# Kernel optimization log

Measured on AMD Instinct MI355X. Metric: run time of the kernel, lower is better.

The kernel has to match this reference:

```python
import jax, jax.numpy as jnp
import numpy as np

EPS = 1e-6

def setup_inputs() -> dict:
    key = jax.random.key(0)
    ks = jax.random.split(key, 8)
    S, B, I, D, L = 1024, 16, 1024, 1024, 2
    std = np.sqrt(2.0 / (5.0 * I))
    inp = {
        "input": jax.random.normal(ks[0], (S, B, I), jnp.float32),
        "h0": jnp.zeros((L, B, D), jnp.float32),
        "extra0": jnp.zeros((L, B, 3 * D), jnp.float32),
        "W0": jax.random.normal(ks[1], (4 * D, I), jnp.float32) * std,
        "b0": jnp.zeros((4 * D,), jnp.float32).at[2 * D:3 * D].set(
            jax.random.uniform(ks[2], (D,), jnp.float32, 3.0, 6.0)),
        "r0": jnp.zeros((4 * D,), jnp.float32),
        "W1": jax.random.normal(ks[3], (4 * D, D), jnp.float32) * std,
        "b1": jnp.zeros((4 * D,), jnp.float32).at[2 * D:3 * D].set(
            jax.random.uniform(ks[4], (D,), jnp.float32, 3.0, 6.0)),
        "r1": jnp.zeros((4 * D,), jnp.float32),
    }
    return inp

def _cell(x, c, n, h, m, W, b, r):
    # x: (B, in), states: (B, D), W: (4D, in), b/r: (4D,)
    D = h.shape[-1]
    pre = x @ W.T + b  # (B, 4D)
    rz, ri, rf, ro = jnp.split(r, 4)
    z_pre = pre[:, 0 * D:1 * D] + rz * h
    i_pre = pre[:, 1 * D:2 * D] + ri * h
    f_pre = pre[:, 2 * D:3 * D] + rf * h
    o_pre = pre[:, 3 * D:4 * D] + ro * h
    z_t = jnp.tanh(z_pre)
    o_t = jax.nn.sigmoid(o_pre)
    m_new = jnp.maximum(f_pre + m, i_pre)
    f_t = jnp.exp(f_pre + m - m_new)
    i_t = jnp.exp(i_pre - m_new)
    c_new = f_t * c + i_t * z_t
    n_new = f_t * n + i_t
    h_new = o_t * (c_new / (jnp.abs(n_new) + EPS))
    return h_new, c_new, n_new, m_new

def _run(input, h0, extra0, params):
    D = h0.shape[-1]
    c0 = extra0[:, :, 0 * D:1 * D]
    n0 = extra0[:, :, 1 * D:2 * D]
    m0 = extra0[:, :, 2 * D:3 * D]

    def step(carry, x_t):
        h, c, n, m = carry  # each (L, B, D)
        x = x_t
        hs, cs, ns, ms = [], [], [], []
        for l, (W, b, r) in enumerate(params):
            h_new, c_new, n_new, m_new = _cell(x, c[l], n[l], h[l], m[l], W, b, r)
            hs.append(h_new); cs.append(c_new); ns.append(n_new); ms.append(m_new)
            x = h_new
        carry = (jnp.stack(hs), jnp.stack(cs), jnp.stack(ns), jnp.stack(ms))
        return carry, x

    (h_f, c_f, n_f, m_f), output = jax.lax.scan(step, (h0, c0, n0, m0), input)
    extra_f = jnp.concatenate([c_f, n_f, m_f], axis=-1)
    return output, h_f, extra_f

def reference(input, h0, extra0, W0, b0, r0, W1, b1, r1):
    params = [(W0, b0, r0), (W1, b1, r1)]
    return _run(input, h0, extra0, params)
```

## Files before the change

### kernel.cpp

```cpp
#include <hip/hip_runtime.h>
#include <hip/hip_bf16.h>

#define S_LEN  1024
#define BATCH  16
#define IDIM   1024
#define DDIM   1024
#define NG     4096
#define BD     16384
#define LAYERS 2
#define PF     16
#define PFP    8
#define NSEG   16

typedef __attribute__((ext_vector_type(8))) short   short8;
typedef __attribute__((ext_vector_type(4))) float   floatx4;
typedef __attribute__((address_space(1))) void      as1_void;
typedef __attribute__((address_space(3))) void      as3_void;

#define L2E  1.4426950408889634f
#define LN2  0.6931471805599453f

#define EXP2F(x) exp2f(x)

static __device__ __forceinline__ unsigned short f2bf(float x) {
    unsigned int u = __float_as_uint(x);
    return (unsigned short)((u + 0x7fffu + ((u >> 16) & 1u)) >> 16);
}

__global__ void detect_dtype(const void* w, int* flag)
{
    const __hip_bfloat16* p = (const __hip_bfloat16*)w;
    float mx = 0.0f;
    for (int i = threadIdx.x; i < 4096; i += 64) {
        float v = __bfloat162float(p[i]);
        float a = fabsf(v);
        if (!(a == a)) a = 1e30f;
        mx = fmaxf(mx, a);
    }
#pragma unroll
    for (int o = 32; o > 0; o >>= 1)
        mx = fmaxf(mx, __shfl_down(mx, o, 64));
    if (threadIdx.x == 0) *flag = (mx > 1e3f) ? 1 : 0;
}

__global__ void to_bf16(const void* src, size_t elem_off, const int* flag,
                        unsigned short* dst, int n)
{
    const int i = blockIdx.x * 256 + threadIdx.x;
    if (i >= n) return;
    if (*flag) dst[i] = f2bf(((const float*)src)[elem_off + i]);
    else       dst[i] = ((const unsigned short*)src)[elem_off + i];
}

__global__ void prep_small(const void* __restrict__ h0,
                           const void* __restrict__ extra0,
                           const void* __restrict__ b0s, const void* __restrict__ r0s,
                           const void* __restrict__ b1s, const void* __restrict__ r1s,
                           const int* __restrict__ flag,
                           float* __restrict__ state,
                           float* __restrict__ pb,
                           int* __restrict__ rflag)
{
    const int blk = blockIdx.x;
    const int fl = *flag;

    if (blk < 128) {
        const int idx = blk * 256 + threadIdx.x;
        const int l  = idx / BD;
        const int bd = idx % BD;
        const int b = bd >> 10, d = bd & 1023;
        float* st = state + (size_t)l * 4 * BD;
        const size_t eoff = ((size_t)l * BATCH + b) * (3 * DDIM);
        float cv, nv, mv, hv;
        if (fl) {
            const float* e = (const float*)extra0 + eoff;
            cv = e[d]; nv = e[DDIM + d]; mv = e[2 * DDIM + d];
            hv = ((const float*)h0)[(size_t)l * BD + bd];
        } else {
            const __hip_bfloat16* e = (const __hip_bfloat16*)extra0 + eoff;
            cv = __bfloat162float(e[d]);
            nv = __bfloat162float(e[DDIM + d]);
            mv = __bfloat162float(e[2 * DDIM + d]);
            hv = __bfloat162float(((const __hip_bfloat16*)h0)[(size_t)l * BD + bd]);
        }
        st[0 * BD + bd] = cv;
        st[1 * BD + bd] = nv;
        st[2 * BD + bd] = mv * L2E;
        st[3 * BD + bd] = hv;
        return;
    }

    const int which = blk - 128;
    const void* src = (which == 0) ? b0s : (which == 1) ? r0s
                    : (which == 2) ? b1s : r1s;
    float* dst = pb + (size_t)which * NG;
    int nz = 0;
#pragma unroll
    for (int j = 0; j < NG / 256; j++) {
        const int i = j * 256 + threadIdx.x;
        float v;
        if (fl) {
            v = ((const float*)src)[i];
            nz |= (v != 0.0f);
        } else {
            const unsigned short u = ((const unsigned short*)src)[i];
            nz |= ((u & 0x7fffu) != 0);
            v = __bfloat162float(((const __hip_bfloat16*)src)[i]);
        }
        dst[i] = v;
    }
    if (which == 1 || which == 3) {
        __shared__ int s[4];
        const int w = threadIdx.x >> 6;
        const int any = __any(nz) ? 1 : 0;
        if ((threadIdx.x & 63) == 0) s[w] = any;
        __syncthreads();
        if (threadIdx.x == 0) rflag[which >> 1] = !(s[0] | s[1] | s[2] | s[3]);
    }
}

__global__ __launch_bounds__(256, 2)
void gemm_bias(const __hip_bfloat16* __restrict__ A,
               const __hip_bfloat16* __restrict__ W,
               const float* __restrict__ bias,
               unsigned short* __restrict__ out,
               const int* __restrict__ rflag, int tpad)
{
    constexpr int K = 1024;
    __shared__ alignas(16) __hip_bfloat16 sA[128 * 32];
    __shared__ alignas(16) __hip_bfloat16 sB[128 * 32];

    const int t  = threadIdx.x;
    const int m0 = blockIdx.y * 128;
    const int nb = blockIdx.x;
    const int lr = t & 15;
    const int q  = (t >> 4) & 3;
    const int w  = t >> 6;
    const int wm = w >> 1, wn = w & 1;
    const int sr = t >> 2;
    const int sk = (t & 3) * 8;

    floatx4 acc[4][4] = {};

    const __hip_bfloat16* Ab = A + (size_t)(m0 + sr) * K + sk;
    const int wrow = ((sr >> 5) << 10) + nb * 32 + (sr & 31);
    const __hip_bfloat16* Wb = W + (size_t)wrow * K + sk;

    for (int k0 = 0; k0 < K; k0 += 32) {
        __syncthreads();
        __builtin_amdgcn_global_load_lds((as1_void*)(Ab + k0),            (as3_void*)&sA[sr * 32 + sk],        16, 0, 0);
        __builtin_amdgcn_global_load_lds((as1_void*)(Ab + 64 * K + k0),   (as3_void*)&sA[(sr + 64) * 32 + sk], 16, 0, 0);
        __builtin_amdgcn_global_load_lds((as1_void*)(Wb + k0),            (as3_void*)&sB[sr * 32 + sk],        16, 0, 0);
        __builtin_amdgcn_global_load_lds((as1_void*)(Wb + 2048 * K + k0), (as3_void*)&sB[(sr + 64) * 32 + sk], 16, 0, 0);
        __syncthreads();

        short8 af[4], bf[4];
#pragma unroll
        for (int i = 0; i < 4; i++)
            af[i] = *(const short8*)&sA[(wm * 64 + i * 16 + lr) * 32 + q * 8];
#pragma unroll
        for (int j = 0; j < 4; j++)
            bf[j] = *(const short8*)&sB[(j * 32 + wn * 16 + lr) * 32 + q * 8];
#pragma unroll
        for (int i = 0; i < 4; i++)
#pragma unroll
            for (int j = 0; j < 4; j++)
                acc[i][j] = __builtin_amdgcn_mfma_f32_16x16x32_bf16(af[i], bf[j], acc[i][j], 0, 0, 0);
    }

    const int d = nb * 32 + wn * 16 + lr;
    const int cl = ((nb & 1) << 5) + wn * 16 + lr;
    const int cbBase = nb >> 1;
    const float sc[4] = {2.0f * L2E, L2E, L2E, L2E};
    float bb[4];
#pragma unroll
    for (int g = 0; g < 4; g++) bb[g] = sc[g] * bias[g * 1024 + d];

    const int rfast = *rflag;

#pragma unroll
    for (int i = 0; i < 4; i++) {
#pragma unroll
        for (int reg = 0; reg < 4; reg++) {
            const int row  = m0 + wm * 64 + i * 16 + q * 4 + reg;
            const int trow = row >> 4;
            const int b    = row & 15;
            float v[4];
#pragma unroll
            for (int g = 0; g < 4; g++)
                v[g] = acc[i][g][reg] * sc[g] + bb[g];
            if (rfast) {
                const float zv = v[0];
                const float e2 = EXP2F(-fabsf(zv));
                v[0] = copysignf((1.0f - e2) * __builtin_amdgcn_rcpf(1.0f + e2), zv);
                v[3] = __builtin_amdgcn_rcpf(1.0f + EXP2F(-v[3]));
            }
            union { unsigned short us[4]; uint2 u2; } pk;
#pragma unroll
            for (int g = 0; g < 4; g++) pk.us[g] = f2bf(v[g]);
            const int cb = b * 16 + cbBase;
            *(uint2*)(out + (((size_t)cb * tpad + trow) * 64 + cl) * 4) = pk.u2;
        }
    }
}

__global__ void scan_passA(const unsigned int* __restrict__ pre,
                           const int* __restrict__ rflag,
                           float* __restrict__ smry, int T, int tpad)
{
    if (!*rflag) return;
    const int gid = blockIdx.x * 256 + threadIdx.x;
    const int chain = gid & (BD - 1);
    const int seg = gid >> 14;
    const int SEG = T / NSEG;
    const int cb = chain >> 6, cl = chain & 63;

    const uint2* p = (const uint2*)pre
                   + ((size_t)cb * tpad + seg * SEG) * 64 + cl;

    float al = 0.0f, mu = -3e38f, Bh = 0.0f, Nh = 0.0f;

    unsigned int k0[PFP], k1[PFP];
#pragma unroll
    for (int u = 0; u < PFP; u++) {
        const uint2 v = p[(size_t)u * 64];
        k0[u] = v.x; k1[u] = v.y;
    }

    for (int t = 0; t < SEG; t += PFP) {
#pragma unroll
        for (int u = 0; u < PFP; u++) {
            const float zt = __uint_as_float(k0[u] << 16);
            const float i2 = __uint_as_float(k0[u] & 0xffff0000u);
            const float f2 = __uint_as_float(k1[u] << 16);

            const uint2 nv = p[(size_t)(t + u + PFP) * 64];
            k0[u] = nv.x; k1[u] = nv.y;

            al += f2;
            const float e  = i2 - al;
            const float mn = fmaxf(mu, e);
            const float s  = EXP2F(mu - mn);
            const float ww = EXP2F(e - mn);
            Bh = fmaf(Bh, s, ww * zt);
            Nh = fmaf(Nh, s, ww);
            mu = mn;
        }
    }

    smry[0 * NSEG * BD + seg * BD + chain] = al;
    smry[1 * NSEG * BD + seg * BD + chain] = al + mu;
    smry[2 * NSEG * BD + seg * BD + chain] = Bh;
    smry[3 * NSEG * BD + seg * BD + chain] = Nh;
}

__global__ void scan_mid(float* __restrict__ smry,
                         const int* __restrict__ rflag,
                         const float* __restrict__ state, int T)
{
    if (!*rflag) return;
    const int idx = blockIdx.x * 256 + threadIdx.x;
    float c  = state[0 * BD + idx];
    float n  = state[1 * BD + idx];
    float m2 = state[2 * BD + idx];
#pragma unroll
    for (int s = 0; s < NSEG; s++) {
        const float A    = smry[0 * NSEG * BD + s * BD + idx];
        const float bmax = smry[1 * NSEG * BD + s * BD + idx];
        const float Bh   = smry[2 * NSEG * BD + s * BD + idx];
        const float Nh   = smry[3 * NSEG * BD + s * BD + idx];
        smry[0 * NSEG * BD + s * BD + idx] = c;
        smry[1 * NSEG * BD + s * BD + idx] = n;
        smry[2 * NSEG * BD + s * BD + idx] = m2;
        const float mn = fmaxf(m2 + A, bmax);
        const float sc = EXP2F(m2 + A - mn);
        const float w  = EXP2F(bmax - mn);
        c  = fmaf(sc, c, w * Bh);
        n  = fmaf(sc, n, w * Nh);
        m2 = mn;
    }
}

template<int MODE>
__global__ void scan_passB(const unsigned int* __restrict__ pre,
                           const float* __restrict__ smry,
                           const int* __restrict__ rflag,
                           float* __restrict__ state,
                           unsigned short* __restrict__ hseq,
                           void* __restrict__ gout, size_t gout_eoff,
                           const int* __restrict__ flag, int T, int tpad)
{
    if (!*rflag) return;
    const int gid = blockIdx.x * 256 + threadIdx.x;
    const int chain = gid & (BD - 1);
    const int seg = gid >> 14;
    const int SEG = T / NSEG;
    const int t0s = seg * SEG;
    const int cb = chain >> 6, cl = chain & 63;
    const int fl = *flag;

    float c  = smry[0 * NSEG * BD + seg * BD + chain];
    float n  = smry[1 * NSEG * BD + seg * BD + chain];
    float m2 = smry[2 * NSEG * BD + seg * BD + chain];

    const uint2* p = (const uint2*)pre
                   + ((size_t)cb * tpad + t0s) * 64 + cl;

    unsigned short* hb = hseq + chain + (size_t)t0s * BD;
    float*          fo = (float*)gout + gout_eoff + chain + (size_t)t0s * BD;
    unsigned short* bo = (unsigned short*)gout + gout_eoff + chain + (size_t)t0s * BD;

    float h = 0.0f;
    unsigned int k0[PFP], k1[PFP];
#pragma unroll
    for (int u = 0; u < PFP; u++) {
        const uint2 v = p[(size_t)u * 64];
        k0[u] = v.x; k1[u] = v.y;
    }

    for (int t = 0; t < SEG; t += PFP) {
#pragma unroll
        for (int u = 0; u < PFP; u++) {
            const float zt = __uint_as_float(k0[u] << 16);
            const float i2 = __uint_as_float(k0[u] & 0xffff0000u);
            const float f2 = __uint_as_float(k1[u] << 16);
            const float ot = __uint_as_float(k1[u] & 0xffff0000u);

            const uint2 nv = p[(size_t)(t + u + PFP) * 64];
            k0[u] = nv.x; k1[u] = nv.y;

            const float fm = f2 + m2;
            const float mn = fmaxf(fm, i2);
            const float ft = EXP2F(fm - mn);
            const float it = EXP2F(i2 - mn);

            c  = fmaf(ft, c, it * zt);
            n  = fmaf(ft, n, it);
            m2 = mn;
            h  = ot * c * __builtin_amdgcn_rcpf(fabsf(n) + 1e-6f);

            const size_t toff = (size_t)(t + u) * BD;
            if (MODE == 0)      hb[toff] = f2bf(h);
            else if (fl)        fo[toff] = h;
            else                bo[toff] = f2bf(h);
        }
    }

    if (seg == NSEG - 1) {
        state[0 * BD + chain] = c;
        state[1 * BD + chain] = n;
        state[2 * BD + chain] = m2;
        state[3 * BD + chain] = h;
    }
}

template<int MODE>
__global__ void slstm_scan(const unsigned int* __restrict__ pre,
                           const float* __restrict__ r,
                           float* __restrict__ state,
                           unsigned short* __restrict__ hseq,
                           void* __restrict__ gout, size_t gout_eoff,
                           const int* __restrict__ flag,
                           const int* __restrict__ rflag, int T, int tpad,
                           int pgate)
{
    const int rfast = *rflag;
    if (pgate && rfast) return;

    const int idx = blockIdx.x * 64 + threadIdx.x;
    const int d = idx & 1023;
    const int cb = idx >> 6, cl = idx & 63;
    const int fl = *flag;

    const float rz = r[d]            * (2.0f * L2E);
    const float ri = r[DDIM + d]     * L2E;
    const float rf = r[2 * DDIM + d] * L2E;
    const float ro = r[3 * DDIM + d] * L2E;

    float c  = state[0 * BD + idx];
    float n  = state[1 * BD + idx];
    float m2 = state[2 * BD + idx];
    float h  = state[3 * BD + idx];

    const uint2* p = (const uint2*)pre + (size_t)cb * tpad * 64 + cl;

    unsigned short* hb = hseq + idx;
    float*          fo = (float*)gout + gout_eoff + idx;
    unsigned short* bo = (unsigned short*)gout + gout_eoff + idx;

    unsigned int k0[PF], k1[PF];
#pragma unroll
    for (int u = 0; u < PF; u++) {
        const uint2 v = p[(size_t)u * 64];
        k0[u] = v.x; k1[u] = v.y;
    }

    if (rfast) {
        for (int t8 = 0; t8 < T; t8 += PF) {
#pragma unroll
            for (int u = 0; u < PF; u++) {
                const float zt = __uint_as_float(k0[u] << 16);
                const float i2 = __uint_as_float(k0[u] & 0xffff0000u);
                const float f2 = __uint_as_float(k1[u] << 16);
                const float ot = __uint_as_float(k1[u] & 0xffff0000u);

                const uint2 nv = p[(size_t)(t8 + u + PF) * 64];
                k0[u] = nv.x; k1[u] = nv.y;

                const float fm = f2 + m2;
                const float mn = fmaxf(fm, i2);
                const float ft = EXP2F(fm - mn);
                const float it = EXP2F(i2 - mn);

                c  = fmaf(ft, c, it * zt);
                n  = fmaf(ft, n, it);
                m2 = mn;
                h  = ot * c * __builtin_amdgcn_rcpf(fabsf(n) + 1e-6f);

                const size_t toff = (size_t)(t8 + u) * BD;
                if (MODE == 0)      hb[toff] = f2bf(h);
                else if (fl)        fo[toff] = h;
                else                bo[toff] = f2bf(h);
            }
        }
    } else {
        for (int t8 = 0; t8 < T; t8 += PF) {
#pragma unroll
            for (int u = 0; u < PF; u++) {
                float z2 = __uint_as_float(k0[u] << 16);
                float i2 = __uint_as_float(k0[u] & 0xffff0000u);
                float f2 = __uint_as_float(k1[u] << 16);
                float o2 = __uint_as_float(k1[u] & 0xffff0000u);

                const uint2 nv = p[(size_t)(t8 + u + PF) * 64];
                k0[u] = nv.x; k1[u] = nv.y;

                z2 = fmaf(rz, h, z2);
                i2 = fmaf(ri, h, i2);
                f2 = fmaf(rf, h, f2);
                o2 = fmaf(ro, h, o2);

                const float fm = f2 + m2;
                const float mn = fmaxf(fm, i2);
                const float ft = EXP2F(fm - mn);
                const float it = EXP2F(i2 - mn);

                const float e2 = EXP2F(-fabsf(z2));
                const float zt = copysignf((1.0f - e2) * __builtin_amdgcn_rcpf(1.0f + e2), z2);
                const float ot = __builtin_amdgcn_rcpf(1.0f + EXP2F(-o2));

                c  = ft * c + it * zt;
                n  = ft * n + it;
                m2 = mn;
                h  = ot * c * __builtin_amdgcn_rcpf(fabsf(n) + 1e-6f);

                const size_t toff = (size_t)(t8 + u) * BD;
                if (MODE == 0)      hb[toff] = f2bf(h);
                else if (fl)        fo[toff] = h;
                else                bo[toff] = f2bf(h);
            }
        }
    }

    state[0 * BD + idx] = c;
    state[1 * BD + idx] = n;
    state[2 * BD + idx] = m2;
    state[3 * BD + idx] = h;
}

__global__ void finalize(const float* __restrict__ state,
                         void* __restrict__ out,
                         const int* __restrict__ flag)
{
    const int idx = blockIdx.x * 256 + threadIdx.x;
    const int l  = idx / BD;
    const int bd = idx % BD;
    const int b = bd >> 10, d = bd & 1023;
    const float* st = state + (size_t)l * 4 * BD;
    const float cv = st[0 * BD + bd], nv = st[1 * BD + bd];
    const float mv = st[2 * BD + bd] * LN2;
    const float hv = st[3 * BD + bd];

    const size_t hoff = (size_t)S_LEN * BD + idx;
    const size_t eoff = (size_t)S_LEN * BD + (size_t)LAYERS * BD
                      + ((size_t)l * BATCH + b) * (3 * DDIM);
    if (*flag) {
        float* o = (float*)out;
        o[hoff] = hv;
        o[eoff + d] = cv; o[eoff + DDIM + d] = nv; o[eoff + 2 * DDIM + d] = mv;
    } else {
        unsigned short* o = (unsigned short*)out;
        o[hoff] = f2bf(hv);
        o[eoff + d]            = f2bf(cv);
        o[eoff + DDIM + d]     = f2bf(nv);
        o[eoff + 2 * DDIM + d] = f2bf(mv);
    }
}

__global__ void zero_out_k(void* __restrict__ out, const int* __restrict__ flag,
                           int out_size)
{
    const size_t i = (size_t)blockIdx.x * 256 + threadIdx.x;
    const size_t nb = (size_t)out_size * ((*flag) ? 4 : 2);
    char* o = (char*)out;
    for (size_t j = i * 4; j < (i + 1) * 4 && j < nb; j++) o[j] = 0;
}

extern "C" void kernel_launch(void* const* d_in, const int* in_sizes, int n_in,
                              void* d_out, int out_size, void* d_ws, size_t ws_size,
                              hipStream_t stream)
{
    const void* input  = d_in[0];
    const void* h0     = d_in[1];
    const void* extra0 = d_in[2];
    const void* W0     = d_in[3];
    const void* b0     = d_in[4];
    const void* r0     = d_in[5];
    const void* W1     = d_in[6];
    const void* b1     = d_in[7];
    const void* r1     = d_in[8];

    const size_t FLAG_B  = 256;
    const size_t STATE_B = (size_t)LAYERS * 4 * BD * 4;
    const size_t W_B     = (size_t)NG * IDIM * 2;
    const size_t PB_B    = (size_t)4 * NG * 4;
    const size_t SM_B    = (size_t)4 * NSEG * BD * 4;
    const size_t FIXED   = FLAG_B + STATE_B + 2 * W_B + PB_B + SM_B;

    int T = 0;
    for (int cand = S_LEN; cand >= 8; cand >>= 1) {
        size_t need = FIXED
                    + (size_t)cand * BD * 2
                    + (size_t)cand * BD * 2
                    + (size_t)(cand + PF) * BD * 8;
        if (need <= ws_size) { T = cand; break; }
    }

    char* ws = (char*)d_ws;
    int*   flag  = (int*)ws;
    int*   rflag = flag + 1;
    float* state = (float*)(ws + FLAG_B);
    __hip_bfloat16* W0b = (__hip_bfloat16*)(ws + FLAG_B + STATE_B);
    __hip_bfloat16* W1b = W0b + (size_t)NG * IDIM;
    float* pb    = (float*)(ws + FLAG_B + STATE_B + 2 * W_B);
    float* b0f = pb, *r0f = pb + NG, *b1f = pb + 2 * NG, *r1f = pb + 3 * NG;
    float* smry  = (float*)(ws + FLAG_B + STATE_B + 2 * W_B + PB_B);
    unsigned short* Ain  = (unsigned short*)(ws + FIXED);
    unsigned short* hseq = Ain + (size_t)T * BD;
    unsigned short* pre  = hseq + (size_t)T * BD;

    detect_dtype<<<dim3(1), dim3(64), 0, stream>>>(W0, flag);

    if (T == 0) {
        zero_out_k<<<dim3((out_size + 255) / 256), dim3(256), 0, stream>>>(d_out, flag, out_size);
        return;
    }

    const int WN = NG * IDIM;
    to_bf16<<<dim3(WN / 256), dim3(256), 0, stream>>>(W0, 0, flag, (unsigned short*)W0b, WN);
    to_bf16<<<dim3(WN / 256), dim3(256), 0, stream>>>(W1, 0, flag, (unsigned short*)W1b, WN);

    prep_small<<<dim3(132), dim3(256), 0, stream>>>(h0, extra0, b0, r0, b1, r1,
                                                    flag, state, pb, rflag);

    const int  tpad = T + PF;
    const dim3 gemmGrid(32, (T * BATCH) / 128);
    const dim3 scanGrid(BD / 64);
    const dim3 passGrid((BD * NSEG) / 256);
    const dim3 midGrid(BD / 256);
    const int  nch = S_LEN / T;
    const int  useP = (T >= 256 && (T % (NSEG * PFP)) == 0) ? 1 : 0;

    for (int ch = 0; ch < nch; ch++) {
        const int t0 = ch * T;

        to_bf16<<<dim3((T * BD) / 256), dim3(256), 0, stream>>>(
            input, (size_t)t0 * BD, flag, Ain, T * BD);

        gemm_bias<<<gemmGrid, 256, 0, stream>>>((const __hip_bfloat16*)Ain, W0b, b0f, pre, rflag + 0, tpad);
        if (useP) {
            scan_passA<<<passGrid, 256, 0, stream>>>((const unsigned int*)pre, rflag + 0, smry, T, tpad);
            scan_mid<<<midGrid, 256, 0, stream>>>(smry, rflag + 0, state, T);
            scan_passB<0><<<passGrid, 256, 0, stream>>>((const unsigned int*)pre, smry, rflag + 0,
                                                        state, hseq, (void*)0, 0, flag, T, tpad);
        }
        slstm_scan<0><<<scanGrid, 64, 0, stream>>>((const unsigned int*)pre, r0f, state,
                                                   hseq, (void*)0, 0, flag, rflag + 0, T, tpad, useP);

        gemm_bias<<<gemmGrid, 256, 0, stream>>>((const __hip_bfloat16*)hseq, W1b, b1f, pre, rflag + 1, tpad);
        if (useP) {
            scan_passA<<<passGrid, 256, 0, stream>>>((const unsigned int*)pre, rflag + 1, smry, T, tpad);
            scan_mid<<<midGrid, 256, 0, stream>>>(smry, rflag + 1, state + 4 * BD, T);
            scan_passB<1><<<passGrid, 256, 0, stream>>>((const unsigned int*)pre, smry, rflag + 1,
                                                        state + 4 * BD, (unsigned short*)0,
                                                        d_out, (size_t)t0 * BD, flag, T, tpad);
        }
        slstm_scan<1><<<scanGrid, 64, 0, stream>>>((const unsigned int*)pre, r1f,
                                                   state + 4 * BD, (unsigned short*)0,
                                                   d_out, (size_t)t0 * BD, flag, rflag + 1, T, tpad, useP);
    }

    finalize<<<dim3(LAYERS * BD / 256), dim3(256), 0, stream>>>(state, d_out, flag);
}
```

Before: 630.6 us.

## Rewrite input-projection GEMM with 256x256 tiles, triple-buffered LDS and swizzle

```diff
diff --git a/kernel.cpp b/kernel.cpp
--- a/kernel.cpp
+++ b/kernel.cpp
@@ -119,58 +119,86 @@
     }
 }
 
-__global__ __launch_bounds__(256, 2)
+__global__ __launch_bounds__(512, 2)
 void gemm_bias(const __hip_bfloat16* __restrict__ A,
                const __hip_bfloat16* __restrict__ W,
                const float* __restrict__ bias,
                unsigned short* __restrict__ out,
                const int* __restrict__ rflag, int tpad)
 {
-    constexpr int K = 1024;
-    __shared__ alignas(16) __hip_bfloat16 sA[128 * 32];
-    __shared__ alignas(16) __hip_bfloat16 sB[128 * 32];
-
-    const int t  = threadIdx.x;
-    const int m0 = blockIdx.y * 128;
-    const int nb = blockIdx.x;
-    const int lr = t & 15;
-    const int q  = (t >> 4) & 3;
-    const int w  = t >> 6;
-    const int wm = w >> 1, wn = w & 1;
-    const int sr = t >> 2;
-    const int sk = (t & 3) * 8;
-
-    floatx4 acc[4][4] = {};
-
-    const __hip_bfloat16* Ab = A + (size_t)(m0 + sr) * K + sk;
-    const int wrow = ((sr >> 5) << 10) + nb * 32 + (sr & 31);
-    const __hip_bfloat16* Wb = W + (size_t)wrow * K + sk;
-
-    for (int k0 = 0; k0 < K; k0 += 32) {
-        __syncthreads();
-        __builtin_amdgcn_global_load_lds((as1_void*)(Ab + k0),            (as3_void*)&sA[sr * 32 + sk],        16, 0, 0);
-        __builtin_amdgcn_global_load_lds((as1_void*)(Ab + 64 * K + k0),   (as3_void*)&sA[(sr + 64) * 32 + sk], 16, 0, 0);
-        __builtin_amdgcn_global_load_lds((as1_void*)(Wb + k0),            (as3_void*)&sB[sr * 32 + sk],        16, 0, 0);
-        __builtin_amdgcn_global_load_lds((as1_void*)(Wb + 2048 * K + k0), (as3_void*)&sB[(sr + 64) * 32 + sk], 16, 0, 0);
-        __syncthreads();
-
-        short8 af[4], bf[4];
-#pragma unroll
-        for (int i = 0; i < 4; i++)
-            af[i] = *(const short8*)&sA[(wm * 64 + i * 16 + lr) * 32 + q * 8];
-#pragma unroll
-        for (int j = 0; j < 4; j++)
-            bf[j] = *(const short8*)&sB[(j * 32 + wn * 16 + lr) * 32 + q * 8];
-#pragma unroll
-        for (int i = 0; i < 4; i++)
-#pragma unroll
-            for (int j = 0; j < 4; j++)
-                acc[i][j] = __builtin_amdgcn_mfma_f32_16x16x32_bf16(af[i], bf[j], acc[i][j], 0, 0, 0);
-    }
-
-    const int d = nb * 32 + wn * 16 + lr;
-    const int cl = ((nb & 1) << 5) + wn * 16 + lr;
-    const int cbBase = nb >> 1;
+    __shared__ alignas(16) __hip_bfloat16 sA[3][256 * 32];
+    __shared__ alignas(16) __hip_bfloat16 sB[3][256 * 32];
+
+    const int t    = threadIdx.x;
+    const int m0   = blockIdx.y * 256;
+    const int nb   = blockIdx.x;
+    const int lane = t & 63;
+    const int lr   = lane & 15;
+    const int q    = lane >> 4;
+    const int w    = t >> 6;
+    const int wm   = w >> 2, wn = w & 3;
+
+    const int srow = t >> 2;
+    const int qd   = t & 3;
+    const int qs   = qd ^ ((srow >> 1) & 3);
+    const __hip_bfloat16* Abase = A + (size_t)(m0 + srow) * 1024 + qs * 8;
+    const int r1   = 128 + srow;
+    const int wr0  = (srow >> 6) * 1024 + nb * 64 + (srow & 63);
+    const int wr1  = (r1 >> 6) * 1024 + nb * 64 + (r1 & 63);
+    const __hip_bfloat16* Wb0 = W + (size_t)wr0 * 1024 + qs * 8;
+    const __hip_bfloat16* Wb1 = W + (size_t)wr1 * 1024 + qs * 8;
+
+    const int rc = q ^ ((lr >> 1) & 3);
+
+    floatx4 acc[8][4] = {};
+
+#define STAGE(bi, kk) do {                                                                                   \
+    __builtin_amdgcn_global_load_lds((as1_void*)(Abase + (kk)),              (as3_void*)&sA[bi][t * 8],        16, 0, 0); \
+    __builtin_amdgcn_global_load_lds((as1_void*)(Abase + 128 * 1024 + (kk)), (as3_void*)&sA[bi][4096 + t * 8], 16, 0, 0); \
+    __builtin_amdgcn_global_load_lds((as1_void*)(Wb0 + (kk)),                (as3_void*)&sB[bi][t * 8],        16, 0, 0); \
+    __builtin_amdgcn_global_load_lds((as1_void*)(Wb1 + (kk)),                (as3_void*)&sB[bi][4096 + t * 8], 16, 0, 0); \
+} while (0)
+
+    STAGE(0, 0);
+    STAGE(1, 32);
+    asm volatile("s_waitcnt vmcnt(4)" ::: "memory");
+    __builtin_amdgcn_s_barrier();
+
+    for (int kt = 0; kt < 32; ++kt) {
+        const int cur = kt % 3;
+        const __hip_bfloat16* cA = sA[cur];
+        const __hip_bfloat16* cB = sB[cur];
+
+        short8 af[8], bf[4];
+#pragma unroll
+        for (int i = 0; i < 8; i++)
+            af[i] = *(const short8*)&cA[(wm * 128 + i * 16 + lr) * 32 + rc * 8];
+#pragma unroll
+        for (int g = 0; g < 4; g++)
+            bf[g] = *(const short8*)&cB[(g * 64 + wn * 16 + lr) * 32 + rc * 8];
+
+        if (kt < 30) {
+            const int stg = (kt + 2) % 3;
+            STAGE(stg, (kt + 2) * 32);
+        }
+
+        asm volatile("s_waitcnt lgkmcnt(0)" ::: "memory");
+        if (kt < 30)      asm volatile("s_waitcnt vmcnt(4)" ::: "memory");
+        else if (kt == 30) asm volatile("s_waitcnt vmcnt(0)" ::: "memory");
+        __builtin_amdgcn_s_barrier();
+
+        __builtin_amdgcn_s_setprio(1);
+#pragma unroll
+        for (int i = 0; i < 8; i++)
+#pragma unroll
+            for (int g = 0; g < 4; g++)
+                acc[i][g] = __builtin_amdgcn_mfma_f32_16x16x32_bf16(af[i], bf[g], acc[i][g], 0, 0, 0);
+        __builtin_amdgcn_s_setprio(0);
+    }
+#undef STAGE
+
+    const int d  = nb * 64 + wn * 16 + lr;
+    const int cl = wn * 16 + lr;
     const float sc[4] = {2.0f * L2E, L2E, L2E, L2E};
     float bb[4];
 #pragma unroll
@@ -179,10 +207,10 @@
     const int rfast = *rflag;
 
 #pragma unroll
-    for (int i = 0; i < 4; i++) {
+    for (int i = 0; i < 8; i++) {
 #pragma unroll
         for (int reg = 0; reg < 4; reg++) {
-            const int row  = m0 + wm * 64 + i * 16 + q * 4 + reg;
+            const int row  = m0 + wm * 128 + i * 16 + q * 4 + reg;
             const int trow = row >> 4;
             const int b    = row & 15;
             float v[4];
@@ -198,7 +226,7 @@
             union { unsigned short us[4]; uint2 u2; } pk;
 #pragma unroll
             for (int g = 0; g < 4; g++) pk.us[g] = f2bf(v[g]);
-            const int cb = b * 16 + cbBase;
+            const int cb = b * 16 + nb;
             *(uint2*)(out + (((size_t)cb * tpad + trow) * 64 + cl) * 4) = pk.u2;
         }
     }
@@ -528,7 +556,7 @@
     const size_t FIXED   = FLAG_B + STATE_B + 2 * W_B + PB_B + SM_B;
 
     int T = 0;
-    for (int cand = S_LEN; cand >= 8; cand >>= 1) {
+    for (int cand = S_LEN; cand >= 16; cand >>= 1) {
         size_t need = FIXED
                     + (size_t)cand * BD * 2
                     + (size_t)cand * BD * 2
@@ -564,7 +592,7 @@
                                                     flag, state, pb, rflag);
 
     const int  tpad = T + PF;
-    const dim3 gemmGrid(32, (T * BATCH) / 128);
+    const dim3 gemmGrid(DDIM / 64, (T * BATCH) / 256);
     const dim3 scanGrid(BD / 64);
     const dim3 passGrid((BD * NSEG) / 256);
     const dim3 midGrid(BD / 256);
@@ -577,7 +605,7 @@
         to_bf16<<<dim3((T * BD) / 256), dim3(256), 0, stream>>>(
             input, (size_t)t0 * BD, flag, Ain, T * BD);
 
-        gemm_bias<<<gemmGrid, 256, 0, stream>>>((const __hip_bfloat16*)Ain, W0b, b0f, pre, rflag + 0, tpad);
+        gemm_bias<<<gemmGrid, 512, 0, stream>>>((const __hip_bfloat16*)Ain, W0b, b0f, pre, rflag + 0, tpad);
         if (useP) {
             scan_passA<<<passGrid, 256, 0, stream>>>((const unsigned int*)pre, rflag + 0, smry, T, tpad);
             scan_mid<<<midGrid, 256, 0, stream>>>(smry, rflag + 0, state, T);
@@ -587,7 +615,7 @@
         slstm_scan<0><<<scanGrid, 64, 0, stream>>>((const unsigned int*)pre, r0f, state,
                                                    hseq, (void*)0, 0, flag, rflag + 0, T, tpad, useP);
 
-        gemm_bias<<<gemmGrid, 256, 0, stream>>>((const __hip_bfloat16*)hseq, W1b, b1f, pre, rflag + 1, tpad);
+        gemm_bias<<<gemmGrid, 512, 0, stream>>>((const __hip_bfloat16*)hseq, W1b, b1f, pre, rflag + 1, tpad);
         if (useP) {
             scan_passA<<<passGrid, 256, 0, stream>>>((const unsigned int*)pre, rflag + 1, smry, T, tpad);
             scan_mid<<<midGrid, 256, 0, stream>>>(smry, rflag + 1, state + 4 * BD, T);
```

New measurement: 594.8 us. 5.7% less time.
